# Optimization experiments

Measured on AMD Instinct MI355X. Metric: run time of the kernel, lower is better.

The kernel has to match this reference:

```python
import jax, jax.numpy as jnp
import numpy as np

HEAD_SIZE = 128  # embeddings_dims // no_of_heads = 4096 // 32


def apply_rope(v):
    # v: [B, S, d] with d = HEAD_SIZE; interleaved-pair rotation as in source
    B, S, d = v.shape
    pos = jnp.arange(S, dtype=jnp.float32)[:, None]              # [S, 1]
    idx = jnp.arange(0, d, 2, dtype=jnp.float32)[None, :]        # [1, d//2]
    theta = jnp.power(10000.0, -2.0 * idx / d)                   # [1, d//2]
    angles = pos * theta                                         # [S, d//2]
    cos = jnp.cos(angles)
    sin = jnp.sin(angles)
    vr = v.reshape(B, S, d // 2, 2)
    x0, x1 = vr[..., 0], vr[..., 1]
    out = jnp.stack([x0 * cos - x1 * sin, x1 * cos + x0 * sin], axis=-1)
    return out.reshape(B, S, d)


def setup_inputs() -> dict:
    key = jax.random.key(0)
    kx, kq, kk, kv = jax.random.split(key, 4)
    B, S, D = 2, 4096, 4096
    d = HEAD_SIZE
    scale = 1.0 / np.sqrt(D)
    return {
        "x": jax.random.normal(kx, (B, S, D), dtype=jnp.float32),
        "Wq": jax.random.normal(kq, (d, D), dtype=jnp.float32) * scale,
        "Wk": jax.random.normal(kk, (d, D), dtype=jnp.float32) * scale,
        "Wv": jax.random.normal(kv, (d, D), dtype=jnp.float32) * scale,
    }


def reference(x, Wq, Wk, Wv):
    # single attention head, non-flash path (eval mode: dropout = identity)
    B, S, D = x.shape
    q = jnp.einsum('bsd,hd->bsh', x, Wq)  # [B, S, head]
    k = jnp.einsum('bsd,hd->bsh', x, Wk)
    v = jnp.einsum('bsd,hd->bsh', x, Wv)
    q = apply_rope(q)
    k = apply_rope(k)
    scale = k.shape[-1] ** (-0.5)
    scores = jnp.einsum('bqh,bkh->bqk', q, k) * scale  # [B, S, S]
    causal = jnp.tril(jnp.ones((S, S), dtype=bool))
    scores = jnp.where(causal, scores, -jnp.inf)
    weights = jax.nn.softmax(scores, axis=-1)
    out = jnp.einsum('bqk,bkh->bqh', weights, v)  # [B, S, head]
    return out
```

## Files before the change

### kernel.cpp

```cpp
#include <hip/hip_runtime.h>

typedef _Float16 half8 __attribute__((ext_vector_type(8)));
typedef _Float16 half2v __attribute__((ext_vector_type(2)));
typedef float f32x4 __attribute__((ext_vector_type(4)));

#define S_LEN 4096
#define D_DIM 4096
#define HD 128


#define ASTR 40
#define QSTR 136
__global__ __launch_bounds__(256) void proj_kernel(const float* __restrict__ x,
                                                   const float* __restrict__ wq,
                                                   const float* __restrict__ wk,
                                                   const float* __restrict__ wv,
                                                   _Float16* __restrict__ qw,
                                                   _Float16* __restrict__ kw,
                                                   _Float16* __restrict__ vt) {
    __shared__ __align__(16) _Float16 smem[17408];
    const int tid = threadIdx.x;
    const int bx = blockIdx.x;
    const int M0 = blockIdx.y * 64;
    const float* w = (bx == 0) ? wq : (bx == 1) ? wk : wv;
    const int lane = tid & 63, wv_ = tid >> 6;
    const int l15 = lane & 15, quad = lane >> 4;

    const int arow = tid >> 2, acol = (tid & 3) * 8;
    const int brow = tid >> 1, bcol = (tid & 1) * 16;
    const float* xa = x + (size_t)(M0 + arow) * D_DIM + acol;
    const float* wb = w + (size_t)brow * D_DIM + bcol;

    f32x4 acc[4][2];
    for (int mi = 0; mi < 4; ++mi)
        for (int ni = 0; ni < 2; ++ni)
            acc[mi][ni] = (f32x4){0.f, 0.f, 0.f, 0.f};

    auto stage = [&](_Float16* Ash, _Float16* Bsh, float4 A0, float4 A1,
                     float4 B0, float4 B1, float4 B2, float4 B3) {
        half8 ha = { (_Float16)A0.x, (_Float16)A0.y, (_Float16)A0.z, (_Float16)A0.w,
                     (_Float16)A1.x, (_Float16)A1.y, (_Float16)A1.z, (_Float16)A1.w };
        half8 hb0 = { (_Float16)B0.x, (_Float16)B0.y, (_Float16)B0.z, (_Float16)B0.w,
                      (_Float16)B1.x, (_Float16)B1.y, (_Float16)B1.z, (_Float16)B1.w };
        half8 hb1 = { (_Float16)B2.x, (_Float16)B2.y, (_Float16)B2.z, (_Float16)B2.w,
                      (_Float16)B3.x, (_Float16)B3.y, (_Float16)B3.z, (_Float16)B3.w };
        *(half8*)&Ash[arow * ASTR + acol] = ha;
        *(half8*)&Bsh[brow * ASTR + bcol] = hb0;
        *(half8*)&Bsh[brow * ASTR + bcol + 8] = hb1;
    };
    auto compute = [&](const _Float16* Ash, const _Float16* Bsh) {
        half8 af[4], bf[2];
        for (int mi = 0; mi < 4; ++mi)
            af[mi] = *(const half8*)&Ash[(mi * 16 + l15) * ASTR + quad * 8];
        for (int ni = 0; ni < 2; ++ni)
            bf[ni] = *(const half8*)&Bsh[(wv_ * 32 + ni * 16 + l15) * ASTR + quad * 8];
        for (int mi = 0; mi < 4; ++mi)
            for (int ni = 0; ni < 2; ++ni)
                acc[mi][ni] = __builtin_amdgcn_mfma_f32_16x16x32_f16(af[mi], bf[ni],
                                                                     acc[mi][ni], 0, 0, 0);
    };

#define LOADSET(Aa, Ab, Ba, Bb, Bc, Bd, off)                                  \
    Aa = *(const float4*)(xa + (off));     Ab = *(const float4*)(xa + (off) + 4);  \
    Ba = *(const float4*)(wb + (off));     Bb = *(const float4*)(wb + (off) + 4);  \
    Bc = *(const float4*)(wb + (off) + 8); Bd = *(const float4*)(wb + (off) + 12);

    float4 a0_0, a0_1, b0_0, b0_1, b0_2, b0_3;
    float4 a1_0, a1_1, b1_0, b1_1, b1_2, b1_3;
    LOADSET(a0_0, a0_1, b0_0, b0_1, b0_2, b0_3, 0)
    LOADSET(a1_0, a1_1, b1_0, b1_1, b1_2, b1_3, 32)

    for (int i = 0; i < 128; i += 2) {
        stage(smem, smem + 2560, a0_0, a0_1, b0_0, b0_1, b0_2, b0_3);
        if (i + 2 < 128) {
            const int off = (i + 2) * 32;
            LOADSET(a0_0, a0_1, b0_0, b0_1, b0_2, b0_3, off)
        }
        __syncthreads();
        compute(smem, smem + 2560);
        stage(smem + 7680, smem + 10240, a1_0, a1_1, b1_0, b1_1, b1_2, b1_3);
        if (i + 3 < 128) {
            const int off = (i + 3) * 32;
            LOADSET(a1_0, a1_1, b1_0, b1_1, b1_2, b1_3, off)
        }
        __syncthreads();
        compute(smem + 7680, smem + 10240);
    }
#undef LOADSET
    __syncthreads();

    if (bx < 2) {
        for (int mi = 0; mi < 4; ++mi)
            for (int ni = 0; ni < 2; ++ni)
                for (int r = 0; r < 4; ++r)
                    smem[(mi * 16 + quad * 4 + r) * QSTR + wv_ * 32 + ni * 16 + l15] =
                        (_Float16)acc[mi][ni][r];
        __syncthreads();
        _Float16* dst = ((bx == 0) ? qw : kw) + (size_t)M0 * HD;
        const int row = tid >> 2, c0 = (tid & 3) * 32;
        for (int j = 0; j < 4; ++j)
            *(half8*)&dst[row * HD + c0 + j * 8] = *(const half8*)&smem[row * QSTR + c0 + j * 8];
    } else {
        for (int mi = 0; mi < 4; ++mi)
            for (int ni = 0; ni < 2; ++ni)
                for (int r = 0; r < 4; ++r)
                    smem[(wv_ * 32 + ni * 16 + l15) * QSTR + mi * 16 + quad * 4 + r] =
                        (_Float16)acc[mi][ni][r];
        __syncthreads();
        _Float16* dst = vt + (size_t)(M0 >> 12) * HD * S_LEN + (M0 & (S_LEN - 1));
        const int hd = tid >> 1, s0 = (tid & 1) * 32;
        for (int j = 0; j < 4; ++j)
            *(half8*)&dst[(size_t)hd * S_LEN + s0 + j * 8] =
                *(const half8*)&smem[hd * QSTR + s0 + j * 8];
    }
}

__global__ __launch_bounds__(256) void rope_kernel(_Float16* __restrict__ qw,
                                                   _Float16* __restrict__ kw) {
    const int g = blockIdx.x * 256 + threadIdx.x;
    const int m = g >> 6, p = g & 63;
    const int s = m & (S_LEN - 1);
    const float theta = exp2f((float)p * -0.4152410118609203f);
    float sn, cn;
    sincosf((float)s * theta, &sn, &cn);
    const size_t off = (size_t)m * HD + 2 * p;
    half2v qv = *(half2v*)&qw[off];
    half2v kv = *(half2v*)&kw[off];
    float q0 = qv[0], q1 = qv[1], k0 = kv[0], k1 = kv[1];
    half2v qo = { (_Float16)(q0 * cn - q1 * sn), (_Float16)(q1 * cn + q0 * sn) };
    half2v ko = { (_Float16)(k0 * cn - k1 * sn), (_Float16)(k1 * cn + k0 * sn) };
    *(half2v*)&qw[off] = qo;
    *(half2v*)&kw[off] = ko;
}

__device__ __forceinline__ void load_kf(const _Float16* __restrict__ kb, int kbase,
                                        int l15, int quad, half8* kf) {
    const _Float16* kr = kb + (size_t)(kbase + l15) * HD + quad * 8;
    for (int kk = 0; kk < 4; ++kk) {
        kf[kk]     = *(const half8*)(kr + kk * 32);
        kf[4 + kk] = *(const half8*)(kr + 16 * HD + kk * 32);
    }
}

template<bool MASKED>
__device__ __forceinline__ void attn_tile(int kbase, int qg, int l15, int quad,
                                          const half8* kf,
                                          const _Float16* __restrict__ vtb,
                                          const half8* bq, f32x4* acc,
                                          float& mrun, float& lrun) {
    const float csc = 0.1275174348796053f;
    f32x4 st0 = (f32x4){0.f, 0.f, 0.f, 0.f};
    f32x4 st1 = (f32x4){0.f, 0.f, 0.f, 0.f};
    for (int kk = 0; kk < 4; ++kk) {
        st0 = __builtin_amdgcn_mfma_f32_16x16x32_f16(kf[kk],     bq[kk], st0, 0, 0, 0);
        st1 = __builtin_amdgcn_mfma_f32_16x16x32_f16(kf[4 + kk], bq[kk], st1, 0, 0, 0);
    }
    half8 va[8];
    const _Float16* vr = vtb + (size_t)l15 * S_LEN + kbase + quad * 8;
    for (int c = 0; c < 8; ++c)
        va[c] = *(const half8*)(vr + (size_t)c * 16 * S_LEN);
    float p0[4], p1[4];
    float mloc = -1e30f;
    for (int r = 0; r < 4; ++r) {
        float v0 = st0[r] * csc;
        float v1 = st1[r] * csc;
        if (MASKED) {
            const int key0 = kbase + quad * 4 + r;
            if (key0 > qg)      v0 = -1e30f;
            if (key0 + 16 > qg) v1 = -1e30f;
        }
        p0[r] = v0; p1[r] = v1;
        mloc = fmaxf(mloc, fmaxf(v0, v1));
    }
    mloc = fmaxf(mloc, __shfl_xor(mloc, 16));
    mloc = fmaxf(mloc, __shfl_xor(mloc, 32));
    const float mnew = fmaxf(mrun, mloc);
    const float alpha = exp2f(mrun - mnew);
    mrun = mnew;
    float ls = 0.f;
    for (int r = 0; r < 4; ++r) {
        p0[r] = exp2f(p0[r] - mnew);
        p1[r] = exp2f(p1[r] - mnew);
        ls += p0[r] + p1[r];
    }
    ls += __shfl_xor(ls, 16);
    ls += __shfl_xor(ls, 32);
    lrun = lrun * alpha + ls;
    for (int c = 0; c < 8; ++c)
        acc[c] *= alpha;
    int ph0 = __builtin_bit_cast(int, __builtin_amdgcn_cvt_pkrtz(p0[0], p0[1]));
    int ph1 = __builtin_bit_cast(int, __builtin_amdgcn_cvt_pkrtz(p0[2], p0[3]));
    int ph2 = __builtin_bit_cast(int, __builtin_amdgcn_cvt_pkrtz(p1[0], p1[1]));
    int ph3 = __builtin_bit_cast(int, __builtin_amdgcn_cvt_pkrtz(p1[2], p1[3]));
    const int s0 = (l15 + (((quad << 1)    ) & 3) * 16) * 4;
    const int s1 = (l15 + (((quad << 1) + 1) & 3) * 16) * 4;
    int a0 = __builtin_amdgcn_ds_bpermute(s0, ph0);
    int a1 = __builtin_amdgcn_ds_bpermute(s0, ph1);
    int a2 = __builtin_amdgcn_ds_bpermute(s1, ph0);
    int a3 = __builtin_amdgcn_ds_bpermute(s1, ph1);
    int b0 = __builtin_amdgcn_ds_bpermute(s0, ph2);
    int b1 = __builtin_amdgcn_ds_bpermute(s0, ph3);
    int b2 = __builtin_amdgcn_ds_bpermute(s1, ph2);
    int b3 = __builtin_amdgcn_ds_bpermute(s1, ph3);
    const bool lo = quad < 2;
    int4 pi = { lo ? a0 : b0, lo ? a1 : b1, lo ? a2 : b2, lo ? a3 : b3 };
    half8 pf = __builtin_bit_cast(half8, pi);
    for (int c = 0; c < 8; ++c)
        acc[c] = __builtin_amdgcn_mfma_f32_16x16x32_f16(va[c], pf, acc[c], 0, 0, 0);
}

__global__ __launch_bounds__(256) void attn_kernel(const _Float16* __restrict__ q,
                                                   const _Float16* __restrict__ k,
                                                   const _Float16* __restrict__ vt,
                                                   float* __restrict__ out) {
    __shared__ __align__(16) float Osh[4][16][132];
    __shared__ float msh[4][16];
    __shared__ float lsh[4][16];
    const int tid = threadIdx.x;
    const int lane = tid & 63, wv_ = tid >> 6;
    const int l15 = lane & 15, quad = lane >> 4;
    const int bidx = blockIdx.x;
    const int b = bidx & 1;
    const int t = 255 - (bidx >> 1);
    const int qb = t * 16;
    const int qg = qb + l15;

    const _Float16* qp = q + (size_t)(b * S_LEN + qb) * HD;
    half8 bq[4];
    for (int kk = 0; kk < 4; ++kk)
        bq[kk] = *(const half8*)&qp[l15 * HD + kk * 32 + quad * 8];

    f32x4 acc[8];
    for (int c = 0; c < 8; ++c) acc[c] = (f32x4){0.f, 0.f, 0.f, 0.f};
    float mrun = -1e30f, lrun = 0.f;

    const _Float16* kb = k + (size_t)b * S_LEN * HD;
    const _Float16* vtb = vt + (size_t)b * HD * S_LEN;

    const int nfull = (qb + 1) >> 5;
    const int kend = nfull * 32;
    const bool hasm = ((nfull & 3) == wv_);
    const int kb0 = wv_ * 32;

    half8 kf[8], kf2[8];
    if (kb0 < kend)      load_kf(kb, kb0, l15, quad, kf);
    else if (hasm)       load_kf(kb, kend, l15, quad, kf);
    for (int kbase = kb0; kbase < kend; kbase += 128) {
        const int kn = kbase + 128;
        if (kn < kend)   load_kf(kb, kn, l15, quad, kf2);
        else if (hasm)   load_kf(kb, kend, l15, quad, kf2);
        attn_tile<false>(kbase, qg, l15, quad, kf, vtb, bq, acc, mrun, lrun);
        for (int j = 0; j < 8; ++j) kf[j] = kf2[j];
    }
    if (hasm)
        attn_tile<true>(kend, qg, l15, quad, kf, vtb, bq, acc, mrun, lrun);

    for (int c = 0; c < 8; ++c)
        *(f32x4*)&Osh[wv_][l15][c * 16 + quad * 4] = acc[c];
    if (quad == 0) { msh[wv_][l15] = mrun; lsh[wv_][l15] = lrun; }
    __syncthreads();

    const int qr = tid >> 4, dg = (tid & 15) * 8;
    float m0 = msh[0][qr], m1 = msh[1][qr], m2 = msh[2][qr], m3 = msh[3][qr];
    float mm = fmaxf(fmaxf(m0, m1), fmaxf(m2, m3));
    float f0 = exp2f(m0 - mm), f1 = exp2f(m1 - mm), f2 = exp2f(m2 - mm), f3 = exp2f(m3 - mm);
    float l = lsh[0][qr] * f0 + lsh[1][qr] * f1 + lsh[2][qr] * f2 + lsh[3][qr] * f3;
    f32x4 oa = (f32x4){0.f, 0.f, 0.f, 0.f}, ob = oa;
    oa += *(f32x4*)&Osh[0][qr][dg] * f0;  ob += *(f32x4*)&Osh[0][qr][dg + 4] * f0;
    oa += *(f32x4*)&Osh[1][qr][dg] * f1;  ob += *(f32x4*)&Osh[1][qr][dg + 4] * f1;
    oa += *(f32x4*)&Osh[2][qr][dg] * f2;  ob += *(f32x4*)&Osh[2][qr][dg + 4] * f2;
    oa += *(f32x4*)&Osh[3][qr][dg] * f3;  ob += *(f32x4*)&Osh[3][qr][dg + 4] * f3;
    const float inv = 1.0f / l;
    float* op = out + (size_t)(b * S_LEN + qb + qr) * HD + dg;
    *(float4*)op       = (float4){oa[0] * inv, oa[1] * inv, oa[2] * inv, oa[3] * inv};
    *(float4*)(op + 4) = (float4){ob[0] * inv, ob[1] * inv, ob[2] * inv, ob[3] * inv};
}

extern "C" void kernel_launch(void* const* d_in, const int* in_sizes, int n_in,
                              void* d_out, int out_size, void* d_ws, size_t ws_size,
                              hipStream_t stream) {
    const float* x  = (const float*)d_in[0];
    const float* Wq = (const float*)d_in[1];
    const float* Wk = (const float*)d_in[2];
    const float* Wv = (const float*)d_in[3];
    float* out = (float*)d_out;
    char* ws = (char*)d_ws;
    _Float16* qw = (_Float16*)(ws);
    _Float16* kw = (_Float16*)(ws + (2u << 20));
    _Float16* vt = (_Float16*)(ws + (4u << 20));

    proj_kernel<<<dim3(3, 128), dim3(256), 0, stream>>>(x, Wq, Wk, Wv, qw, kw, vt);
    rope_kernel<<<dim3(2048), dim3(256), 0, stream>>>(qw, kw);
    attn_kernel<<<dim3(512), dim3(256), 0, stream>>>(qw, kw, vt, out);
}
```

Before: 364.1 us.

## Fuse RoPE into projection epilogue, halve M tile, swizzle grid for more blocks

Removes the separate rope kernel and applies the rotary rotation to Q and K in the projection epilogue, before they are written out. This saves one launch and a read-modify-write pass over Q and K. The projection M tile shrinks from 64 to 32 rows, so the grid goes from 384 to 768 blocks on a 1D launch. A swizzle groups blocks so that those sharing an x tile (q/k/v) are scheduled near each other. Smaller tiles give more parallelism across CUs but less weight reuse per block, and they re-read the weight matrices more often.

```diff
diff --git a/kernel.cpp b/kernel.cpp
--- a/kernel.cpp
+++ b/kernel.cpp
@@ -1,6 +1,7 @@
 #include <hip/hip_runtime.h>
 
 typedef _Float16 half8 __attribute__((ext_vector_type(8)));
+typedef _Float16 half4 __attribute__((ext_vector_type(4)));
 typedef _Float16 half2v __attribute__((ext_vector_type(2)));
 typedef float f32x4 __attribute__((ext_vector_type(4)));
 
@@ -18,119 +19,124 @@
                                                    _Float16* __restrict__ qw,
                                                    _Float16* __restrict__ kw,
                                                    _Float16* __restrict__ vt) {
-    __shared__ __align__(16) _Float16 smem[17408];
+    __shared__ __align__(16) _Float16 smem[12800];
     const int tid = threadIdx.x;
-    const int bx = blockIdx.x;
-    const int M0 = blockIdx.y * 64;
+    const int wg = blockIdx.x;
+    const int swz = (wg & 7) * 96 + (wg >> 3);
+    const int bx = swz % 3;
+    const int M0 = (swz / 3) * 32;
     const float* w = (bx == 0) ? wq : (bx == 1) ? wk : wv;
     const int lane = tid & 63, wv_ = tid >> 6;
     const int l15 = lane & 15, quad = lane >> 4;
 
-    const int arow = tid >> 2, acol = (tid & 3) * 8;
+    const int arow = tid >> 3, acol = (tid & 7) * 4;
     const int brow = tid >> 1, bcol = (tid & 1) * 16;
     const float* xa = x + (size_t)(M0 + arow) * D_DIM + acol;
     const float* wb = w + (size_t)brow * D_DIM + bcol;
 
-    f32x4 acc[4][2];
-    for (int mi = 0; mi < 4; ++mi)
+    f32x4 acc[2][2];
+    for (int mi = 0; mi < 2; ++mi)
         for (int ni = 0; ni < 2; ++ni)
             acc[mi][ni] = (f32x4){0.f, 0.f, 0.f, 0.f};
 
-    auto stage = [&](_Float16* Ash, _Float16* Bsh, float4 A0, float4 A1,
+    auto stage = [&](_Float16* Ash, _Float16* Bsh, float4 A0,
                      float4 B0, float4 B1, float4 B2, float4 B3) {
-        half8 ha = { (_Float16)A0.x, (_Float16)A0.y, (_Float16)A0.z, (_Float16)A0.w,
-                     (_Float16)A1.x, (_Float16)A1.y, (_Float16)A1.z, (_Float16)A1.w };
+        half4 ha = { (_Float16)A0.x, (_Float16)A0.y, (_Float16)A0.z, (_Float16)A0.w };
         half8 hb0 = { (_Float16)B0.x, (_Float16)B0.y, (_Float16)B0.z, (_Float16)B0.w,
                       (_Float16)B1.x, (_Float16)B1.y, (_Float16)B1.z, (_Float16)B1.w };
         half8 hb1 = { (_Float16)B2.x, (_Float16)B2.y, (_Float16)B2.z, (_Float16)B2.w,
                       (_Float16)B3.x, (_Float16)B3.y, (_Float16)B3.z, (_Float16)B3.w };
-        *(half8*)&Ash[arow * ASTR + acol] = ha;
+        *(half4*)&Ash[arow * ASTR + acol] = ha;
         *(half8*)&Bsh[brow * ASTR + bcol] = hb0;
         *(half8*)&Bsh[brow * ASTR + bcol + 8] = hb1;
     };
     auto compute = [&](const _Float16* Ash, const _Float16* Bsh) {
-        half8 af[4], bf[2];
-        for (int mi = 0; mi < 4; ++mi)
+        half8 af[2], bf[2];
+        for (int mi = 0; mi < 2; ++mi)
             af[mi] = *(const half8*)&Ash[(mi * 16 + l15) * ASTR + quad * 8];
         for (int ni = 0; ni < 2; ++ni)
             bf[ni] = *(const half8*)&Bsh[(wv_ * 32 + ni * 16 + l15) * ASTR + quad * 8];
-        for (int mi = 0; mi < 4; ++mi)
+        for (int mi = 0; mi < 2; ++mi)
             for (int ni = 0; ni < 2; ++ni)
                 acc[mi][ni] = __builtin_amdgcn_mfma_f32_16x16x32_f16(af[mi], bf[ni],
                                                                      acc[mi][ni], 0, 0, 0);
     };
 
-#define LOADSET(Aa, Ab, Ba, Bb, Bc, Bd, off)                                  \
-    Aa = *(const float4*)(xa + (off));     Ab = *(const float4*)(xa + (off) + 4);  \
-    Ba = *(const float4*)(wb + (off));     Bb = *(const float4*)(wb + (off) + 4);  \
-    Bc = *(const float4*)(wb + (off) + 8); Bd = *(const float4*)(wb + (off) + 12);
-
-    float4 a0_0, a0_1, b0_0, b0_1, b0_2, b0_3;
-    float4 a1_0, a1_1, b1_0, b1_1, b1_2, b1_3;
-    LOADSET(a0_0, a0_1, b0_0, b0_1, b0_2, b0_3, 0)
-    LOADSET(a1_0, a1_1, b1_0, b1_1, b1_2, b1_3, 32)
+#define LOADSET(Aa, Ba, Bb, Bc, Bd, off)                                            \
+    Aa = *(const float4*)(xa + (off));                                              \
+    Ba = *(const float4*)(wb + (off));      Bb = *(const float4*)(wb + (off) + 4);  \
+    Bc = *(const float4*)(wb + (off) + 8);  Bd = *(const float4*)(wb + (off) + 12);
+
+    float4 a0_0, b0_0, b0_1, b0_2, b0_3;
+    float4 a1_0, b1_0, b1_1, b1_2, b1_3;
+    LOADSET(a0_0, b0_0, b0_1, b0_2, b0_3, 0)
+    LOADSET(a1_0, b1_0, b1_1, b1_2, b1_3, 32)
 
     for (int i = 0; i < 128; i += 2) {
-        stage(smem, smem + 2560, a0_0, a0_1, b0_0, b0_1, b0_2, b0_3);
+        stage(smem, smem + 1280, a0_0, b0_0, b0_1, b0_2, b0_3);
         if (i + 2 < 128) {
             const int off = (i + 2) * 32;
-            LOADSET(a0_0, a0_1, b0_0, b0_1, b0_2, b0_3, off)
+            LOADSET(a0_0, b0_0, b0_1, b0_2, b0_3, off)
         }
         __syncthreads();
-        compute(smem, smem + 2560);
-        stage(smem + 7680, smem + 10240, a1_0, a1_1, b1_0, b1_1, b1_2, b1_3);
+        compute(smem, smem + 1280);
+        stage(smem + 6400, smem + 7680, a1_0, b1_0, b1_1, b1_2, b1_3);
         if (i + 3 < 128) {
             const int off = (i + 3) * 32;
-            LOADSET(a1_0, a1_1, b1_0, b1_1, b1_2, b1_3, off)
+            LOADSET(a1_0, b1_0, b1_1, b1_2, b1_3, off)
         }
         __syncthreads();
-        compute(smem + 7680, smem + 10240);
+        compute(smem + 6400, smem + 7680);
     }
 #undef LOADSET
     __syncthreads();
 
     if (bx < 2) {
-        for (int mi = 0; mi < 4; ++mi)
+        for (int mi = 0; mi < 2; ++mi)
             for (int ni = 0; ni < 2; ++ni)
                 for (int r = 0; r < 4; ++r)
                     smem[(mi * 16 + quad * 4 + r) * QSTR + wv_ * 32 + ni * 16 + l15] =
                         (_Float16)acc[mi][ni][r];
         __syncthreads();
         _Float16* dst = ((bx == 0) ? qw : kw) + (size_t)M0 * HD;
-        const int row = tid >> 2, c0 = (tid & 3) * 32;
-        for (int j = 0; j < 4; ++j)
-            *(half8*)&dst[row * HD + c0 + j * 8] = *(const half8*)&smem[row * QSTR + c0 + j * 8];
+        const int row = tid >> 3, c0 = (tid & 7) * 16;
+        const int s = (M0 + row) & (S_LEN - 1);
+        half8 h0 = *(const half8*)&smem[row * QSTR + c0];
+        half8 h1 = *(const half8*)&smem[row * QSTR + c0 + 8];
+        half8 o0, o1;
+        for (int j = 0; j < 4; ++j) {
+            const int p = (c0 >> 1) + j;
+            const float theta = exp2f((float)p * -0.4152410118609203f);
+            float sn, cn;
+            sincosf((float)s * theta, &sn, &cn);
+            const float e0 = (float)h0[2 * j], e1 = (float)h0[2 * j + 1];
+            o0[2 * j]     = (_Float16)(e0 * cn - e1 * sn);
+            o0[2 * j + 1] = (_Float16)(e1 * cn + e0 * sn);
+        }
+        for (int j = 0; j < 4; ++j) {
+            const int p = (c0 >> 1) + 4 + j;
+            const float theta = exp2f((float)p * -0.4152410118609203f);
+            float sn, cn;
+            sincosf((float)s * theta, &sn, &cn);
+            const float e0 = (float)h1[2 * j], e1 = (float)h1[2 * j + 1];
+            o1[2 * j]     = (_Float16)(e0 * cn - e1 * sn);
+            o1[2 * j + 1] = (_Float16)(e1 * cn + e0 * sn);
+        }
+        *(half8*)&dst[row * HD + c0] = o0;
+        *(half8*)&dst[row * HD + c0 + 8] = o1;
     } else {
-        for (int mi = 0; mi < 4; ++mi)
+        for (int mi = 0; mi < 2; ++mi)
             for (int ni = 0; ni < 2; ++ni)
                 for (int r = 0; r < 4; ++r)
-                    smem[(wv_ * 32 + ni * 16 + l15) * QSTR + mi * 16 + quad * 4 + r] =
+                    smem[(wv_ * 32 + ni * 16 + l15) * 40 + mi * 16 + quad * 4 + r] =
                         (_Float16)acc[mi][ni][r];
         __syncthreads();
         _Float16* dst = vt + (size_t)(M0 >> 12) * HD * S_LEN + (M0 & (S_LEN - 1));
-        const int hd = tid >> 1, s0 = (tid & 1) * 32;
-        for (int j = 0; j < 4; ++j)
+        const int hd = tid >> 1, s0 = (tid & 1) * 16;
+        for (int j = 0; j < 2; ++j)
             *(half8*)&dst[(size_t)hd * S_LEN + s0 + j * 8] =
-                *(const half8*)&smem[hd * QSTR + s0 + j * 8];
-    }
-}
-
-__global__ __launch_bounds__(256) void rope_kernel(_Float16* __restrict__ qw,
-                                                   _Float16* __restrict__ kw) {
-    const int g = blockIdx.x * 256 + threadIdx.x;
-    const int m = g >> 6, p = g & 63;
-    const int s = m & (S_LEN - 1);
-    const float theta = exp2f((float)p * -0.4152410118609203f);
-    float sn, cn;
-    sincosf((float)s * theta, &sn, &cn);
-    const size_t off = (size_t)m * HD + 2 * p;
-    half2v qv = *(half2v*)&qw[off];
-    half2v kv = *(half2v*)&kw[off];
-    float q0 = qv[0], q1 = qv[1], k0 = kv[0], k1 = kv[1];
-    half2v qo = { (_Float16)(q0 * cn - q1 * sn), (_Float16)(q1 * cn + q0 * sn) };
-    half2v ko = { (_Float16)(k0 * cn - k1 * sn), (_Float16)(k1 * cn + k0 * sn) };
-    *(half2v*)&qw[off] = qo;
-    *(half2v*)&kw[off] = ko;
+                *(const half8*)&smem[hd * 40 + s0 + j * 8];
+    }
 }
 
 __device__ __forceinline__ void load_kf(const _Float16* __restrict__ kb, int kbase,
@@ -289,7 +295,6 @@
     _Float16* kw = (_Float16*)(ws + (2u << 20));
     _Float16* vt = (_Float16*)(ws + (4u << 20));
 
-    proj_kernel<<<dim3(3, 128), dim3(256), 0, stream>>>(x, Wq, Wk, Wv, qw, kw, vt);
-    rope_kernel<<<dim3(2048), dim3(256), 0, stream>>>(qw, kw);
+    proj_kernel<<<dim3(768), dim3(256), 0, stream>>>(x, Wq, Wk, Wv, qw, kw, vt);
     attn_kernel<<<dim3(512), dim3(256), 0, stream>>>(qw, kw, vt, out);
 }
```

After: 405.6 us. 1.11x slower.

## Split-K the QKV projection with a combine kernel that fuses RoPE and V transpose

Applied to the files above, without the earlier changes.

The projection GEMM is split in two along the reduction dimension, so 768 workgroups run instead of 384. This fills more of the GPU's compute units, and a block-index swizzle groups blocks that share inputs. Each half writes fp32 partials to workspace. A new combine kernel sums them, applies RoPE to Q/K and writes V transposed, replacing the separate rope kernel. The V loads in the attention tile are also hoisted ahead of the QK MFMAs. The trade-off is extra fp32 partial traffic of about 25 MB and one extra launch, with a fallback to the old path when the workspace is too small.

```diff
diff --git a/kernel.cpp b/kernel.cpp
--- a/kernel.cpp
+++ b/kernel.cpp
@@ -11,25 +11,33 @@
 
 #define ASTR 40
 #define QSTR 136
+template<int KSPLIT>
 __global__ __launch_bounds__(256) void proj_kernel(const float* __restrict__ x,
                                                    const float* __restrict__ wq,
                                                    const float* __restrict__ wk,
                                                    const float* __restrict__ wv,
                                                    _Float16* __restrict__ qw,
                                                    _Float16* __restrict__ kw,
-                                                   _Float16* __restrict__ vt) {
+                                                   _Float16* __restrict__ vt,
+                                                   float* __restrict__ P) {
     __shared__ __align__(16) _Float16 smem[17408];
     const int tid = threadIdx.x;
-    const int bx = blockIdx.x;
-    const int M0 = blockIdx.y * 64;
+    const int wg = blockIdx.x;
+    const int nwg = 384 * KSPLIT;
+    const int swz = (wg & 7) * (nwg >> 3) + (wg >> 3);
+    const int bx = swz % 3;
+    const int rest = swz / 3;
+    const int ks = (KSPLIT == 2) ? (rest & 1) : 0;
+    const int M0 = ((KSPLIT == 2) ? (rest >> 1) : rest) * 64;
+    const int NS = 128 / KSPLIT;
     const float* w = (bx == 0) ? wq : (bx == 1) ? wk : wv;
     const int lane = tid & 63, wv_ = tid >> 6;
     const int l15 = lane & 15, quad = lane >> 4;
 
     const int arow = tid >> 2, acol = (tid & 3) * 8;
     const int brow = tid >> 1, bcol = (tid & 1) * 16;
-    const float* xa = x + (size_t)(M0 + arow) * D_DIM + acol;
-    const float* wb = w + (size_t)brow * D_DIM + bcol;
+    const float* xa = x + (size_t)(M0 + arow) * D_DIM + acol + ks * (D_DIM / 2);
+    const float* wb = w + (size_t)brow * D_DIM + bcol + ks * (D_DIM / 2);
 
     f32x4 acc[4][2];
     for (int mi = 0; mi < 4; ++mi)
@@ -70,16 +78,16 @@
     LOADSET(a0_0, a0_1, b0_0, b0_1, b0_2, b0_3, 0)
     LOADSET(a1_0, a1_1, b1_0, b1_1, b1_2, b1_3, 32)
 
-    for (int i = 0; i < 128; i += 2) {
+    for (int i = 0; i < NS; i += 2) {
         stage(smem, smem + 2560, a0_0, a0_1, b0_0, b0_1, b0_2, b0_3);
-        if (i + 2 < 128) {
+        if (i + 2 < NS) {
             const int off = (i + 2) * 32;
             LOADSET(a0_0, a0_1, b0_0, b0_1, b0_2, b0_3, off)
         }
         __syncthreads();
         compute(smem, smem + 2560);
         stage(smem + 7680, smem + 10240, a1_0, a1_1, b1_0, b1_1, b1_2, b1_3);
-        if (i + 3 < 128) {
+        if (i + 3 < NS) {
             const int off = (i + 3) * 32;
             LOADSET(a1_0, a1_1, b1_0, b1_1, b1_2, b1_3, off)
         }
@@ -89,7 +97,19 @@
 #undef LOADSET
     __syncthreads();
 
-    if (bx < 2) {
+    if (KSPLIT == 2) {
+        float* sf = (float*)smem;
+        for (int mi = 0; mi < 4; ++mi)
+            for (int ni = 0; ni < 2; ++ni)
+                for (int r = 0; r < 4; ++r)
+                    sf[(mi * 16 + quad * 4 + r) * 132 + wv_ * 32 + ni * 16 + l15] =
+                        acc[mi][ni][r];
+        __syncthreads();
+        const int row = tid >> 2, c0 = (tid & 3) * 32;
+        float* dst = P + ((size_t)(ks * 3 + bx) * 8192 + M0 + row) * HD + c0;
+        for (int j = 0; j < 8; ++j)
+            *(float4*)(dst + j * 4) = *(const float4*)&sf[row * 132 + c0 + j * 4];
+    } else if (bx < 2) {
         for (int mi = 0; mi < 4; ++mi)
             for (int ni = 0; ni < 2; ++ni)
                 for (int r = 0; r < 4; ++r)
@@ -112,6 +132,74 @@
         for (int j = 0; j < 4; ++j)
             *(half8*)&dst[(size_t)hd * S_LEN + s0 + j * 8] =
                 *(const half8*)&smem[hd * QSTR + s0 + j * 8];
+    }
+}
+
+__global__ __launch_bounds__(256) void combine_kernel(const float* __restrict__ P,
+                                                      _Float16* __restrict__ qw,
+                                                      _Float16* __restrict__ kw,
+                                                      _Float16* __restrict__ vt) {
+    const int tid = threadIdx.x;
+    const int M0 = blockIdx.x * 64;
+    const int row = tid >> 2, c0 = (tid & 3) * 32;
+    if (blockIdx.y == 0) {
+        const float* Pq0 = P + ((size_t)0 * 8192 + M0 + row) * HD + c0;
+        const float* Pq1 = P + ((size_t)3 * 8192 + M0 + row) * HD + c0;
+        const float* Pk0 = P + ((size_t)1 * 8192 + M0 + row) * HD + c0;
+        const float* Pk1 = P + ((size_t)4 * 8192 + M0 + row) * HD + c0;
+        float qv[32], kv[32];
+#pragma unroll
+        for (int j = 0; j < 8; ++j) {
+            float4 a = *(const float4*)(Pq0 + j * 4);
+            float4 b = *(const float4*)(Pq1 + j * 4);
+            float4 c = *(const float4*)(Pk0 + j * 4);
+            float4 d = *(const float4*)(Pk1 + j * 4);
+            qv[j * 4 + 0] = a.x + b.x; qv[j * 4 + 1] = a.y + b.y;
+            qv[j * 4 + 2] = a.z + b.z; qv[j * 4 + 3] = a.w + b.w;
+            kv[j * 4 + 0] = c.x + d.x; kv[j * 4 + 1] = c.y + d.y;
+            kv[j * 4 + 2] = c.z + d.z; kv[j * 4 + 3] = c.w + d.w;
+        }
+        const int s = (M0 + row) & (S_LEN - 1);
+        half8 oq[4], ok[4];
+#pragma unroll
+        for (int jp = 0; jp < 16; ++jp) {
+            const int pi = (c0 >> 1) + jp;
+            const float theta = exp2f((float)pi * -0.4152410118609203f);
+            float sn, cn;
+            sincosf((float)s * theta, &sn, &cn);
+            const float q0 = qv[2 * jp], q1 = qv[2 * jp + 1];
+            const float k0 = kv[2 * jp], k1 = kv[2 * jp + 1];
+            oq[jp >> 2][(2 * jp) & 7]     = (_Float16)(q0 * cn - q1 * sn);
+            oq[jp >> 2][(2 * jp + 1) & 7] = (_Float16)(q1 * cn + q0 * sn);
+            ok[jp >> 2][(2 * jp) & 7]     = (_Float16)(k0 * cn - k1 * sn);
+            ok[jp >> 2][(2 * jp + 1) & 7] = (_Float16)(k1 * cn + k0 * sn);
+        }
+        _Float16* qdst = qw + (size_t)(M0 + row) * HD + c0;
+        _Float16* kdst = kw + (size_t)(M0 + row) * HD + c0;
+#pragma unroll
+        for (int j = 0; j < 4; ++j) {
+            *(half8*)(qdst + j * 8) = oq[j];
+            *(half8*)(kdst + j * 8) = ok[j];
+        }
+    } else {
+        __shared__ __align__(16) _Float16 sh[128][72];
+        const float* Pv0 = P + ((size_t)2 * 8192 + M0 + row) * HD + c0;
+        const float* Pv1 = P + ((size_t)5 * 8192 + M0 + row) * HD + c0;
+#pragma unroll
+        for (int j = 0; j < 8; ++j) {
+            float4 a = *(const float4*)(Pv0 + j * 4);
+            float4 b = *(const float4*)(Pv1 + j * 4);
+            sh[c0 + j * 4 + 0][row] = (_Float16)(a.x + b.x);
+            sh[c0 + j * 4 + 1][row] = (_Float16)(a.y + b.y);
+            sh[c0 + j * 4 + 2][row] = (_Float16)(a.z + b.z);
+            sh[c0 + j * 4 + 3][row] = (_Float16)(a.w + b.w);
+        }
+        __syncthreads();
+        const int hd = tid >> 1, s0 = (tid & 1) * 32;
+        _Float16* dst = vt + (size_t)(M0 >> 12) * HD * S_LEN + (size_t)hd * S_LEN +
+                        (M0 & (S_LEN - 1)) + s0;
+        for (int j = 0; j < 4; ++j)
+            *(half8*)(dst + j * 8) = *(const half8*)&sh[hd][s0 + j * 8];
     }
 }
 
@@ -149,16 +237,16 @@
                                           const half8* bq, f32x4* acc,
                                           float& mrun, float& lrun) {
     const float csc = 0.1275174348796053f;
+    half8 va[8];
+    const _Float16* vr = vtb + (size_t)l15 * S_LEN + kbase + quad * 8;
+    for (int c = 0; c < 8; ++c)
+        va[c] = *(const half8*)(vr + (size_t)c * 16 * S_LEN);
     f32x4 st0 = (f32x4){0.f, 0.f, 0.f, 0.f};
     f32x4 st1 = (f32x4){0.f, 0.f, 0.f, 0.f};
     for (int kk = 0; kk < 4; ++kk) {
         st0 = __builtin_amdgcn_mfma_f32_16x16x32_f16(kf[kk],     bq[kk], st0, 0, 0, 0);
         st1 = __builtin_amdgcn_mfma_f32_16x16x32_f16(kf[4 + kk], bq[kk], st1, 0, 0, 0);
     }
-    half8 va[8];
-    const _Float16* vr = vtb + (size_t)l15 * S_LEN + kbase + quad * 8;
-    for (int c = 0; c < 8; ++c)
-        va[c] = *(const half8*)(vr + (size_t)c * 16 * S_LEN);
     float p0[4], p1[4];
     float mloc = -1e30f;
     for (int r = 0; r < 4; ++r) {
@@ -288,8 +376,15 @@
     _Float16* qw = (_Float16*)(ws);
     _Float16* kw = (_Float16*)(ws + (2u << 20));
     _Float16* vt = (_Float16*)(ws + (4u << 20));
-
-    proj_kernel<<<dim3(3, 128), dim3(256), 0, stream>>>(x, Wq, Wk, Wv, qw, kw, vt);
-    rope_kernel<<<dim3(2048), dim3(256), 0, stream>>>(qw, kw);
+    float* P = (float*)(ws + (6u << 20));
+
+    const size_t need = (size_t)(6u << 20) + (size_t)2 * 3 * 8192 * 128 * 4;
+    if (ws_size >= need) {
+        proj_kernel<2><<<dim3(768), dim3(256), 0, stream>>>(x, Wq, Wk, Wv, qw, kw, vt, P);
+        combine_kernel<<<dim3(128, 2), dim3(256), 0, stream>>>(P, qw, kw, vt);
+    } else {
+        proj_kernel<1><<<dim3(384), dim3(256), 0, stream>>>(x, Wq, Wk, Wv, qw, kw, vt, P);
+        rope_kernel<<<dim3(2048), dim3(256), 0, stream>>>(qw, kw);
+    }
     attn_kernel<<<dim3(512), dim3(256), 0, stream>>>(qw, kw, vt, out);
 }
```

After: 366.1 us. About the same (+0.6%).
